# Optimization experiments

Hardware: AMD Instinct MI355X
Metric: run time of the kernel (lower is better)

The kernel has to match this reference:

```python
import jax, jax.numpy as jnp
import numpy as np

ANCHOR_RADIUS = 5.0


def setup_inputs() -> dict:
    key = jax.random.key(0)
    k1, k2, k3 = jax.random.split(key, 3)
    B, N, E, S = 4, 1024, 32, 2
    embedding = jax.random.normal(k1, (B, N, E), dtype=jnp.float32)
    abs_coords = 10.0 * jax.random.normal(k2, (B, N, S), dtype=jnp.float32)
    patch_mask = jax.random.bernoulli(k3, 0.5, (B, N, N))  # bool [B,N,N]
    return {"embedding": embedding, "abs_coords": abs_coords, "patch_mask": patch_mask}


def reference(embedding, abs_coords, patch_mask):
    B, N, E = embedding.shape
    # pairwise coordinate and embedding differences
    coord_diff = abs_coords[:, :, None, :] - abs_coords[:, None, :, :]   # [B,N,N,2]
    diff = embedding[:, :, None, :] - embedding[:, None, :, :]           # [B,N,N,E]
    diff = diff.at[..., :2].add(coord_diff)
    ssq = jnp.sum(diff * diff, axis=-1)                                   # [B,N,N]
    # safe sqrt: zero grad at zero distance (matches torch norm subgradient)
    dist = jnp.where(ssq == 0, 0.0, jnp.sqrt(jnp.where(ssq == 0, 1.0, ssq)))
    sim = 1.0 - jax.nn.sigmoid(dist * 5.0 / ANCHOR_RADIUS - 5.0)          # [B,N,N]

    # negatives: sim with positive-pair mask and diagonal set to -inf
    eye = jnp.eye(N, dtype=bool)
    neg_mask = patch_mask | eye
    neg_masked = jnp.where(neg_mask, -jnp.inf, sim)                       # [B,N,N]
    lse_neg = jax.scipy.special.logsumexp(neg_masked, axis=-1)            # [B,N]

    # For each positive pair (b,i,j) with patch_mask[b,i,j]:
    #   logits = [sim[b,i,j], neg_masked[b,i,:]] ; CE target=0 ->
    #   loss_contrib = logaddexp(sim[b,i,j], lse_neg[b,i]) - sim[b,i,j]
    lse_tot = jnp.logaddexp(sim, lse_neg[:, :, None])                     # [B,N,N]
    loss = jnp.sum(jnp.where(patch_mask, lse_tot - sim, 0.0))
    return loss
```

## Files before the change

kernel.cpp:

```cpp
#include <hip/hip_runtime.h>

#define BBATCH 4
#define NN 1024
#define EE 32

typedef short v8s __attribute__((ext_vector_type(8)));
typedef float v4f __attribute__((ext_vector_type(4)));

__device__ __forceinline__ unsigned short f32_to_bf16(float v) {
    unsigned u = __builtin_bit_cast(unsigned, v);
    u += 0x7fffu + ((u >> 16) & 1u);
    return (unsigned short)(u >> 16);
}

__global__ __launch_bounds__(256) void prep_kernel(
    const float* __restrict__ emb, const float* __restrict__ coords,
    unsigned short* __restrict__ ybf, float* __restrict__ nrm)
{
    const int g  = blockIdx.x * 256 + threadIdx.x;
    const int r  = g >> 3, qq = g & 7;
    float4 v = ((const float4*)emb)[g];
    if (qq == 0) { v.x += coords[r * 2 + 0]; v.y += coords[r * 2 + 1]; }
    ushort4 h;
    h.x = f32_to_bf16(v.x); h.y = f32_to_bf16(v.y);
    h.z = f32_to_bf16(v.z); h.w = f32_to_bf16(v.w);
    ((ushort4*)ybf)[g] = h;
    float p = v.x * v.x + v.y * v.y + v.z * v.z + v.w * v.w;
    #pragma unroll
    for (int off = 1; off < 8; off <<= 1) p += __shfl_xor(p, off, 64);
    if (qq == 0) nrm[r] = p;
}

__global__ __launch_bounds__(1024) void fused_kernel(
    const unsigned short* __restrict__ ybf, const float* __restrict__ nrm,
    const int* __restrict__ mask, float* __restrict__ out)
{
    const int bid = blockIdx.x;
    const int is = bid & 63;
    const int b  = bid >> 6;
    const int tid  = threadIdx.x;
    const int wave = tid >> 6, lane = tid & 63;
    const int m = lane & 15, q = lane >> 4;

    __shared__ float sums_w[16][16];
    __shared__ float total_s[16];
    __shared__ float wred[16];

    const unsigned short* Y  = ybf + (size_t)b * NN * EE;
    const float*          NR = nrm + b * NN;
    const int i0   = is * 16;
    const int irow = i0 + q * 4;

    const v8s af = *(const v8s*)(Y + (i0 + m) * EE + q * 8);
    float ni[4];
    #pragma unroll
    for (int r = 0; r < 4; ++r) ni[r] = NR[irow + r];

    const int jbase = wave * 64;
    float    ex[4][4];
    float    s[4] = {0.f, 0.f, 0.f, 0.f};
    unsigned mbits = 0u;

    #pragma unroll
    for (int t = 0; t < 4; ++t) {
        const int j0 = jbase + t * 16;
        const v8s bfv = *(const v8s*)(Y + (j0 + m) * EE + q * 8);
        const float njv = NR[j0 + m];
        int mk[4];
        #pragma unroll
        for (int r = 0; r < 4; ++r)
            mk[r] = mask[((size_t)(b * NN + irow + r) << 10) + j0 + m];
        v4f d = __builtin_amdgcn_mfma_f32_16x16x32_bf16(af, bfv, (v4f){0,0,0,0}, 0, 0, 0);
        #pragma unroll
        for (int r = 0; r < 4; ++r) {
            float nn   = ni[r] + njv;
            float ssq  = fmaxf(fmaf(-2.f, d[r], nn), 0.f);
            float dist = __builtin_amdgcn_sqrtf(ssq);
            float sm   = __builtin_amdgcn_rcpf(1.f + __expf(dist - 5.f));
            const float e = __expf(mk[r] != 0 ? -sm : sm);
            ex[t][r] = e;
            bool negm = (mk[r] != 0) || (irow + r == j0 + m);
            s[r] += negm ? 0.f : e;
            if (mk[r] != 0) mbits |= 1u << (t * 4 + r);
        }
    }

    #pragma unroll
    for (int r = 0; r < 4; ++r) {
        float v = s[r];
        #pragma unroll
        for (int off = 8; off > 0; off >>= 1) v += __shfl_down(v, off, 16);
        if (m == 0) sums_w[wave][q * 4 + r] = v;
    }
    __syncthreads();
    if (tid < 16) {
        float tot = 0.f;
        #pragma unroll
        for (int w = 0; w < 16; ++w) tot += sums_w[w][tid];
        total_s[tid] = tot;
    }
    __syncthreads();

    float tot[4];
    #pragma unroll
    for (int r = 0; r < 4; ++r) tot[r] = total_s[q * 4 + r];
    float acc = 0.f;
    #pragma unroll
    for (int t = 0; t < 4; ++t)
        #pragma unroll
        for (int r = 0; r < 4; ++r) {
            float lg = __logf(fmaf(tot[r], ex[t][r], 1.f));
            acc += ((mbits >> (t * 4 + r)) & 1u) ? lg : 0.f;
        }

    #pragma unroll
    for (int off = 32; off > 0; off >>= 1) acc += __shfl_down(acc, off, 64);
    if (lane == 0) wred[wave] = acc;
    __syncthreads();
    if (tid == 0) {
        float a = 0.f;
        #pragma unroll
        for (int w = 0; w < 16; ++w) a += wred[w];
        atomicAdd(out, a);
    }
}

extern "C" void kernel_launch(void* const* d_in, const int* in_sizes, int n_in,
                              void* d_out, int out_size, void* d_ws, size_t ws_size,
                              hipStream_t stream) {
    const float* emb    = (const float*)d_in[0];
    const float* coords = (const float*)d_in[1];
    const int*   mask   = (const int*)d_in[2];
    float*       out    = (float*)d_out;

    unsigned short* ybf = (unsigned short*)d_ws;
    float*          nrv = (float*)((char*)d_ws + BBATCH * NN * EE * 2);

    hipMemsetAsync(out, 0, sizeof(float), stream);
    prep_kernel<<<(BBATCH * NN * EE / 4) / 256, 256, 0, stream>>>(emb, coords, ybf, nrv);
    fused_kernel<<<BBATCH * (NN / 16), 1024, 0, stream>>>(ybf, nrv, mask, out);
}
```

Before: 79.20 us.

## Merge memset, prep and main kernel into one cooperative launch

Replaces the memset plus two kernel launches with a single cooperative kernel that does the bf16/norm prep, zeroes the output, performs a grid-wide sync, then runs the main pairwise computation. The goal is to remove launch and inter-kernel gaps. A fallback path with two regular kernels runs if the cooperative launch fails. The grid sync adds its own barrier cost and needs all 256 blocks of 1024 threads to be co-resident.

```diff
diff --git a/kernel.cpp b/kernel.cpp
--- a/kernel.cpp
+++ b/kernel.cpp
@@ -1,4 +1,7 @@
 #include <hip/hip_runtime.h>
+#include <hip/hip_cooperative_groups.h>
+
+namespace cg = cooperative_groups;
 
 #define BBATCH 4
 #define NN 1024
@@ -13,11 +16,10 @@
     return (unsigned short)(u >> 16);
 }
 
-__global__ __launch_bounds__(256) void prep_kernel(
+__device__ __forceinline__ void prep_work(int g,
     const float* __restrict__ emb, const float* __restrict__ coords,
     unsigned short* __restrict__ ybf, float* __restrict__ nrm)
 {
-    const int g  = blockIdx.x * 256 + threadIdx.x;
     const int r  = g >> 3, qq = g & 7;
     float4 v = ((const float4*)emb)[g];
     if (qq == 0) { v.x += coords[r * 2 + 0]; v.y += coords[r * 2 + 1]; }
@@ -31,20 +33,15 @@
     if (qq == 0) nrm[r] = p;
 }
 
-__global__ __launch_bounds__(1024) void fused_kernel(
+__device__ __forceinline__ void compute_block(int bid, int tid,
     const unsigned short* __restrict__ ybf, const float* __restrict__ nrm,
-    const int* __restrict__ mask, float* __restrict__ out)
+    const int* __restrict__ mask, float* __restrict__ out,
+    float (*sums_w)[16], float* total_s, float* wred)
 {
-    const int bid = blockIdx.x;
     const int is = bid & 63;
     const int b  = bid >> 6;
-    const int tid  = threadIdx.x;
     const int wave = tid >> 6, lane = tid & 63;
     const int m = lane & 15, q = lane >> 4;
-
-    __shared__ float sums_w[16][16];
-    __shared__ float total_s[16];
-    __shared__ float wred[16];
 
     const unsigned short* Y  = ybf + (size_t)b * NN * EE;
     const float*          NR = nrm + b * NN;
@@ -125,6 +122,44 @@
     }
 }
 
+__global__ __launch_bounds__(1024) void fused_coop(
+    const float* __restrict__ emb, const float* __restrict__ coords,
+    const int* __restrict__ mask, float* __restrict__ out,
+    unsigned short* __restrict__ ybf, float* __restrict__ nrm)
+{
+    __shared__ float sums_w[16][16];
+    __shared__ float total_s[16];
+    __shared__ float wred[16];
+
+    const int g = blockIdx.x * 1024 + threadIdx.x;
+    if (g < BBATCH * NN * EE / 4) prep_work(g, emb, coords, ybf, nrm);
+    if (g == 0) out[0] = 0.f;
+    cg::this_grid().sync();
+    compute_block(blockIdx.x, threadIdx.x, ybf, nrm, mask, out,
+                  sums_w, total_s, wred);
+}
+
+__global__ __launch_bounds__(1024) void prep_z_kernel(
+    const float* __restrict__ emb, const float* __restrict__ coords,
+    unsigned short* __restrict__ ybf, float* __restrict__ nrm,
+    float* __restrict__ out)
+{
+    const int g = blockIdx.x * 1024 + threadIdx.x;
+    prep_work(g, emb, coords, ybf, nrm);
+    if (g == 0) out[0] = 0.f;
+}
+
+__global__ __launch_bounds__(1024) void fused_kernel(
+    const unsigned short* __restrict__ ybf, const float* __restrict__ nrm,
+    const int* __restrict__ mask, float* __restrict__ out)
+{
+    __shared__ float sums_w[16][16];
+    __shared__ float total_s[16];
+    __shared__ float wred[16];
+    compute_block(blockIdx.x, threadIdx.x, ybf, nrm, mask, out,
+                  sums_w, total_s, wred);
+}
+
 extern "C" void kernel_launch(void* const* d_in, const int* in_sizes, int n_in,
                               void* d_out, int out_size, void* d_ws, size_t ws_size,
                               hipStream_t stream) {
@@ -136,7 +171,14 @@
     unsigned short* ybf = (unsigned short*)d_ws;
     float*          nrv = (float*)((char*)d_ws + BBATCH * NN * EE * 2);
 
-    hipMemsetAsync(out, 0, sizeof(float), stream);
-    prep_kernel<<<(BBATCH * NN * EE / 4) / 256, 256, 0, stream>>>(emb, coords, ybf, nrv);
-    fused_kernel<<<BBATCH * (NN / 16), 1024, 0, stream>>>(ybf, nrv, mask, out);
+    void* kargs[] = {(void*)&emb, (void*)&coords, (void*)&mask,
+                     (void*)&out, (void*)&ybf, (void*)&nrv};
+    hipError_t e = hipLaunchCooperativeKernel(
+        reinterpret_cast<void*>(fused_coop),
+        dim3(BBATCH * (NN / 16)), dim3(1024), kargs, 0, stream);
+    if (e != hipSuccess) {
+        (void)hipGetLastError();
+        prep_z_kernel<<<32, 1024, 0, stream>>>(emb, coords, ybf, nrv, out);
+        fused_kernel<<<BBATCH * (NN / 16), 1024, 0, stream>>>(ybf, nrv, mask, out);
+    }
 }
```

Result: slower. 115.3 us (+45.6%).
